# Kernel tuning notes

Measured on AMD Instinct MI355X. Metric: run time of the kernel, lower is better.

## Reference

```python
import jax, jax.numpy as jnp
import numpy as np

N = 20000
E = 320000
IN_DIM = 512
HID = 64
HEADS = 8
OUT_DIM = 40
NEG_SLOPE = 0.2


def glorot(key, shape):
    fan = shape[0] + shape[-1] if len(shape) > 1 else shape[-1]
    s = jnp.sqrt(6.0 / fan)
    return jax.random.uniform(key, shape, jnp.float32, -s, s)


def setup_inputs() -> dict:
    key = jax.random.key(0)
    ks = jax.random.split(key, 12)
    x = jax.random.normal(ks[0], (N, IN_DIM), jnp.float32)
    edge_index = jax.random.randint(ks[1], (2, E), 0, N, jnp.int64)
    return {
        "x": x,
        "edge_index": edge_index,
        "W1": glorot(ks[2], (IN_DIM, HEADS * HID)),
        "att1_src": glorot(ks[3], (HEADS, HID)),
        "att1_dst": glorot(ks[4], (HEADS, HID)),
        "b1": jnp.zeros((HEADS * HID,), jnp.float32),
        "W2": glorot(ks[5], (HEADS * HID, HEADS * HID)),
        "att2_src": glorot(ks[6], (HEADS, HID)),
        "att2_dst": glorot(ks[7], (HEADS, HID)),
        "b2": jnp.zeros((HEADS * HID,), jnp.float32),
        "W3": glorot(ks[8], (HEADS * HID, OUT_DIM)),
        "att3_src": glorot(ks[9], (1, OUT_DIM)),
        "att3_dst": glorot(ks[10], (1, OUT_DIM)),
        "b3": jnp.zeros((OUT_DIM,), jnp.float32),
    }


def gat_conv(x, src, dst, W, att_src, att_dst, bias, heads, out_c):
    # h: [N, H, C] transformed node features
    h = (x @ W).reshape(N, heads, out_c)
    a_src = jnp.sum(h * att_src, axis=-1)  # [N, H]
    a_dst = jnp.sum(h * att_dst, axis=-1)  # [N, H]
    # edge logits (message j=src -> i=dst), softmax grouped by dst
    logits = jax.nn.leaky_relu(a_src[src] + a_dst[dst], NEG_SLOPE)  # [Etot, H]
    seg_max = jax.ops.segment_max(logits, dst, num_segments=N)
    seg_max = jnp.where(jnp.isfinite(seg_max), seg_max, 0.0)
    ex = jnp.exp(logits - seg_max[dst])
    denom = jax.ops.segment_sum(ex, dst, num_segments=N)
    alpha = ex / (denom[dst] + 1e-16)  # [Etot, H]
    msg = h[src] * alpha[:, :, None]  # [Etot, H, C]
    out = jax.ops.segment_sum(msg, dst, num_segments=N)  # [N, H, C]
    return out.reshape(N, heads * out_c) + bias


def reference(x, edge_index, W1, att1_src, att1_dst, b1,
              W2, att2_src, att2_dst, b2,
              W3, att3_src, att3_dst, b3):
    # add self loops (PyG GATConv default)
    loops = jnp.arange(N, dtype=edge_index.dtype)
    src = jnp.concatenate([edge_index[0], loops])
    dst = jnp.concatenate([edge_index[1], loops])
    # dropout layers are identity in eval mode
    h = jax.nn.elu(gat_conv(x, src, dst, W1, att1_src, att1_dst, b1, HEADS, HID))
    h = jax.nn.elu(gat_conv(h, src, dst, W2, att2_src, att2_dst, b2, HEADS, HID))
    h = gat_conv(h, src, dst, W3, att3_src, att3_dst, b3, 1, OUT_DIM)
    return jax.nn.log_softmax(h, axis=-1)
```

## Files before the change

kernel.cpp:

```cpp
#include <hip/hip_runtime.h>
#include <math.h>

#define NN 20000
#define EE 320000
#define ETOT (EE + NN)
#define NEG 0.2f

typedef unsigned short ushortT;
typedef __attribute__((ext_vector_type(8))) short short8v;
typedef __attribute__((ext_vector_type(8))) unsigned short u16x8;
typedef __attribute__((ext_vector_type(4))) float f32x4;

__device__ __forceinline__ ushortT f2b(float f){
  unsigned u = __float_as_uint(f);
  u += 0x7FFFu + ((u >> 16) & 1u);
  return (ushortT)(u >> 16);
}
__device__ __forceinline__ float b2f(ushortT b){
  return __uint_as_float(((unsigned)b) << 16);
}

__global__ void k_cvt(const float* __restrict__ in, ushortT* __restrict__ outp, int n4){
  int i = blockIdx.x*blockDim.x + threadIdx.x;
  if(i < n4){
    float4 v = *reinterpret_cast<const float4*>(in + (size_t)i*4);
    ushort4 o;
    o.x = f2b(v.x); o.y = f2b(v.y); o.z = f2b(v.z); o.w = f2b(v.w);
    *reinterpret_cast<ushort4*>(outp + (size_t)i*4) = o;
  }
}

__global__ void k_wtrans(const float* __restrict__ W, ushortT* __restrict__ Wt){
  __shared__ float t[32][33];
  int bk = blockIdx.x*32, bn = blockIdx.y*32;
  int tx = threadIdx.x & 31, ty = threadIdx.x >> 5;
  for(int r=0;r<32;r+=8)
    t[ty+r][tx] = W[(size_t)(bk+ty+r)*512 + bn+tx];
  __syncthreads();
  for(int r=0;r<32;r+=8)
    Wt[(size_t)(bn+ty+r)*512 + bk+tx] = f2b(t[tx][ty+r]);
}

__global__ void k_wtrans3(const float* __restrict__ W3, ushortT* __restrict__ Wt3p){
  int idx = blockIdx.x*blockDim.x + threadIdx.x;
  if(idx >= 64*48*8) return;
  int kslot = idx / 384;
  int rem = idx - kslot*384;
  int n = rem >> 3;
  int jj = rem & 7;
  int k = kslot*8 + jj;
  float v = (n < 40) ? W3[(size_t)k*40 + n] : 0.f;
  Wt3p[idx] = f2b(v);
}

__global__ void k_count(const int* __restrict__ edst, int* __restrict__ counts){
  int e = blockIdx.x*blockDim.x + threadIdx.x;
  if(e < ETOT){
    int d = (e < EE) ? edst[e] : (e - EE);
    atomicAdd(&counts[d], 1);
  }
}

__global__ void k_scan(const int* __restrict__ counts, int* __restrict__ rowstart){
  __shared__ int lds[1024];
  int tid = threadIdx.x;
  int base = tid*20;
  int s = 0;
  for(int j=0;j<20;j++){ int i=base+j; if(i<NN) s += counts[i]; }
  lds[tid] = s; __syncthreads();
  for(int off=1; off<1024; off<<=1){
    int v = (tid>=off) ? lds[tid-off] : 0;
    __syncthreads();
    lds[tid] += v;
    __syncthreads();
  }
  int run = lds[tid] - s;
  for(int j=0;j<20;j++){
    int i = base+j;
    if(i <= NN){
      rowstart[i] = run;
      if(i < NN) run += counts[i];
    }
  }
}

__global__ void k_fill(const int* __restrict__ esrc, const int* __restrict__ edst,
                       const int* __restrict__ rowstart,
                       int* __restrict__ cursor, int* __restrict__ srcs){
  int e = blockIdx.x*blockDim.x + threadIdx.x;
  if(e < ETOT){
    int d = (e < EE) ? edst[e] : (e - EE);
    int s = (e < EE) ? esrc[e] : (e - EE);
    int pos = rowstart[d] + atomicAdd(&cursor[d], 1);
    srcs[pos] = s;
  }
}

__global__ __launch_bounds__(256) void k_gemm_bf16(
    const ushortT* __restrict__ A, const ushortT* __restrict__ Bt,
    ushortT* __restrict__ Cb, int M)
{
  const int K = 512;
  __shared__ __align__(16) ushortT As[128*32];
  __shared__ __align__(16) ushortT Bs[128*32];
  int bm = blockIdx.x*128, bn = blockIdx.y*128;
  int tid = threadIdx.x, wave = tid>>6, lane = tid&63;
  int wm = (wave>>1)*64, wn = (wave&1)*64;
  f32x4 acc[4][4] = {};

  int l4 = lane>>2;
  int s4 = lane&3;
  int src_slot = s4 ^ (l4 & 3);
  int r16 = lane&15, kg = lane>>4;

  for(int k0=0;k0<K;k0+=32){
    #pragma unroll
    for(int c=0;c<2;c++){
      int chunk = wave*2 + c;
      int arow = bm + chunk*16 + l4; if(arow > M-1) arow = M-1;
      const ushortT* ga = A + (size_t)arow*K + k0 + src_slot*8;
      __builtin_amdgcn_global_load_lds(
          (const __attribute__((address_space(1))) void*)ga,
          (__attribute__((address_space(3))) void*)(As + chunk*16*32), 16, 0, 0);
      int brow = bn + chunk*16 + l4;
      const ushortT* gb = Bt + (size_t)brow*K + k0 + src_slot*8;
      __builtin_amdgcn_global_load_lds(
          (const __attribute__((address_space(1))) void*)gb,
          (__attribute__((address_space(3))) void*)(Bs + chunk*16*32), 16, 0, 0);
    }
    asm volatile("s_waitcnt vmcnt(0)");
    __syncthreads();

    short8v a_frag[4], b_frag[4];
    #pragma unroll
    for(int i=0;i<4;i++){
      int row = wm + i*16 + r16;
      a_frag[i] = *reinterpret_cast<const short8v*>(As + row*32 + ((kg ^ (row&3))<<3));
    }
    #pragma unroll
    for(int j=0;j<4;j++){
      int row = wn + j*16 + r16;
      b_frag[j] = *reinterpret_cast<const short8v*>(Bs + row*32 + ((kg ^ (row&3))<<3));
    }
    #pragma unroll
    for(int i=0;i<4;i++)
      #pragma unroll
      for(int j=0;j<4;j++)
        acc[i][j] = __builtin_amdgcn_mfma_f32_16x16x32_bf16(a_frag[i], b_frag[j], acc[i][j], 0, 0, 0);
    __syncthreads();
  }

  #pragma unroll
  for(int i=0;i<4;i++){
    #pragma unroll
    for(int j=0;j<4;j++){
      #pragma unroll
      for(int r=0;r<4;r++){
        int row = bm + wm + i*16 + kg*4 + r;
        int col = bn + wn + j*16 + r16;
        if(row < M) Cb[(size_t)row*512 + col] = f2b(acc[i][j][r]);
      }
    }
  }
}

__global__ __launch_bounds__(256) void k_gemm3m(const ushortT* __restrict__ A,
                                                const ushortT* __restrict__ Wt3p,
                                                float* __restrict__ C, int M){
  const int K = 512;
  __shared__ __align__(16) ushortT As[128*32];
  __shared__ __align__(16) ushortT Bs[64*48*8];
  int bm = blockIdx.x*128;
  int tid = threadIdx.x, wave = tid>>6, lane = tid&63;

  #pragma unroll
  for(int it=0; it<12; it++){
    int o = (it*256 + tid)*8;
    *reinterpret_cast<u16x8*>(Bs + o) = *reinterpret_cast<const u16x8*>(Wt3p + o);
  }

  int l4 = lane>>2, s4 = lane&3;
  int src_slot = s4 ^ (l4 & 3);
  int r16 = lane&15, kg = lane>>4;
  f32x4 acc[2][3] = {};

  for(int k0=0;k0<K;k0+=32){
    #pragma unroll
    for(int c=0;c<2;c++){
      int chunk = wave*2 + c;
      int arow = bm + chunk*16 + l4; if(arow > M-1) arow = M-1;
      const ushortT* ga = A + (size_t)arow*K + k0 + src_slot*8;
      __builtin_amdgcn_global_load_lds(
          (const __attribute__((address_space(1))) void*)ga,
          (__attribute__((address_space(3))) void*)(As + chunk*16*32), 16, 0, 0);
    }
    asm volatile("s_waitcnt vmcnt(0)");
    __syncthreads();

    short8v a_frag[2], b_frag[3];
    #pragma unroll
    for(int i=0;i<2;i++){
      int row = wave*32 + i*16 + r16;
      a_frag[i] = *reinterpret_cast<const short8v*>(As + row*32 + ((kg ^ (row&3))<<3));
    }
    int kslot = (k0>>3) + kg;
    #pragma unroll
    for(int j=0;j<3;j++){
      b_frag[j] = *reinterpret_cast<const short8v*>(Bs + kslot*384 + (j*16 + r16)*8);
    }
    #pragma unroll
    for(int i=0;i<2;i++)
      #pragma unroll
      for(int j=0;j<3;j++)
        acc[i][j] = __builtin_amdgcn_mfma_f32_16x16x32_bf16(a_frag[i], b_frag[j], acc[i][j], 0, 0, 0);
    __syncthreads();
  }

  #pragma unroll
  for(int i=0;i<2;i++){
    #pragma unroll
    for(int j=0;j<3;j++){
      #pragma unroll
      for(int r=0;r<4;r++){
        int row = bm + wave*32 + i*16 + kg*4 + r;
        int col = j*16 + r16;
        if(row < M && col < 40) C[(size_t)row*40 + col] = acc[i][j][r];
      }
    }
  }
}

__global__ void k_attn8(const ushortT* __restrict__ feat, const float* __restrict__ atts,
                        const float* __restrict__ attd, float* __restrict__ a_s,
                        float* __restrict__ a_d){
  int n = blockIdx.x*4 + (threadIdx.x>>6);
  int lane = threadIdx.x & 63;
  if(n >= NN) return;
  int c0 = lane*8;
  u16x8 v = *reinterpret_cast<const u16x8*>(feat + (size_t)n*512 + c0);
  float s1 = 0.f, s2 = 0.f;
  #pragma unroll
  for(int j=0;j<8;j++){
    float f = b2f((ushortT)v[j]);
    s1 += f*atts[c0+j];
    s2 += f*attd[c0+j];
  }
  #pragma unroll
  for(int off=1; off<8; off<<=1){
    s1 += __shfl_xor(s1, off);
    s2 += __shfl_xor(s2, off);
  }
  if((lane&7) == 0){
    int head = lane>>3;
    a_s[n*8+head] = s1;
    a_d[n*8+head] = s2;
  }
}

template<int H, int C>
__global__ void k_attn_f(const float* __restrict__ feat, const float* __restrict__ atts,
                         const float* __restrict__ attd, float* __restrict__ a_s,
                         float* __restrict__ a_d){
  int n = blockIdx.x*4 + (threadIdx.x>>6);
  int lane = threadIdx.x & 63;
  if(n >= NN) return;
  #pragma unroll
  for(int h=0;h<H;h++){
    float s1 = 0.f, s2 = 0.f;
    if(lane < C){
      float v = feat[(size_t)n*(H*C) + h*C + lane];
      s1 = v*atts[h*C+lane];
      s2 = v*attd[h*C+lane];
    }
    for(int off=32; off; off>>=1){
      s1 += __shfl_xor(s1, off);
      s2 += __shfl_xor(s2, off);
    }
    if(lane == 0){ a_s[n*H+h] = s1; a_d[n*H+h] = s2; }
  }
}

__global__ __launch_bounds__(256) void k_agg512(const ushortT* __restrict__ feat,
    const float* __restrict__ a_s, const float* __restrict__ a_d,
    const int* __restrict__ rowstart, const int* __restrict__ srcs,
    const float* __restrict__ bias, ushortT* __restrict__ outb){
  int d = blockIdx.x*4 + (threadIdx.x>>6);
  int lane = threadIdx.x & 63;
  unsigned c0 = (unsigned)lane*8u;
  int head = lane>>3;
  float ad_h = a_d[(size_t)d*8 + head];
  float acc[8] = {0.f,0.f,0.f,0.f,0.f,0.f,0.f,0.f};
  float dsum = 0.f;
  int p0 = rowstart[d], p1 = rowstart[d+1];
  int p = p0;

  for(; p+8 <= p1; p += 8){
    int   ss[8];
    float ll[8];
    u16x8 vv[8];
    #pragma unroll
    for(int q=0;q<8;q++) ss[q] = srcs[p+q];
    #pragma unroll
    for(int q=0;q<8;q++) ll[q] = a_s[((unsigned)ss[q]<<3) + (unsigned)head];
    #pragma unroll
    for(int q=0;q<8;q++) vv[q] = *reinterpret_cast<const u16x8*>(feat + (((unsigned)ss[q]<<9) + c0));
    #pragma unroll
    for(int q=0;q<8;q++){
      float l  = ll[q] + ad_h;
      float al = __expf(fmaxf(l, NEG*l));
      dsum += al;
      #pragma unroll
      for(int j=0;j<8;j++) acc[j] += al*b2f((ushortT)vv[q][j]);
    }
  }
  for(; p+4 <= p1; p += 4){
    int   ss[4];
    float ll[4];
    u16x8 vv[4];
    #pragma unroll
    for(int q=0;q<4;q++) ss[q] = srcs[p+q];
    #pragma unroll
    for(int q=0;q<4;q++) ll[q] = a_s[((unsigned)ss[q]<<3) + (unsigned)head];
    #pragma unroll
    for(int q=0;q<4;q++) vv[q] = *reinterpret_cast<const u16x8*>(feat + (((unsigned)ss[q]<<9) + c0));
    #pragma unroll
    for(int q=0;q<4;q++){
      float l  = ll[q] + ad_h;
      float al = __expf(fmaxf(l, NEG*l));
      dsum += al;
      #pragma unroll
      for(int j=0;j<8;j++) acc[j] += al*b2f((ushortT)vv[q][j]);
    }
  }
  for(; p<p1; p++){
    int s_ = srcs[p];
    float l = a_s[((unsigned)s_<<3) + (unsigned)head] + ad_h;
    u16x8 v = *reinterpret_cast<const u16x8*>(feat + (((unsigned)s_<<9) + c0));
    float al = __expf(fmaxf(l, NEG*l));
    dsum += al;
    #pragma unroll
    for(int j=0;j<8;j++) acc[j] += al*b2f((ushortT)v[j]);
  }

  float invd = 1.f/(dsum + 1e-16f);
  u16x8 ov;
  #pragma unroll
  for(int j=0;j<8;j++){
    float o = acc[j]*invd + bias[c0+j];
    o = (o > 0.f) ? o : (__expf(o) - 1.f);
    ov[j] = f2b(o);
  }
  *reinterpret_cast<u16x8*>(outb + (size_t)d*512 + c0) = ov;
}

__global__ void k_agg_l3(const float* __restrict__ feat,
    const float* __restrict__ a_s, const float* __restrict__ a_d,
    const int* __restrict__ rowstart, const int* __restrict__ srcs,
    const float* __restrict__ bias, float* __restrict__ outp){
  int d = blockIdx.x;
  int lane = threadIdx.x;
  bool act = lane < 40;
  int li = act ? lane : 0;
  float ad_v = a_d[d];
  float acc = 0.f, dsum = 0.f;
  int p0 = rowstart[d], p1 = rowstart[d+1];
  int p = p0;
  for(; p+4 <= p1; p += 4){
    int s0_ = srcs[p], s1_ = srcs[p+1], s2_ = srcs[p+2], s3_ = srcs[p+3];
    float l0 = a_s[s0_] + ad_v, l1 = a_s[s1_] + ad_v;
    float l2 = a_s[s2_] + ad_v, l3 = a_s[s3_] + ad_v;
    float v0 = feat[(size_t)s0_*40 + li];
    float v1 = feat[(size_t)s1_*40 + li];
    float v2 = feat[(size_t)s2_*40 + li];
    float v3 = feat[(size_t)s3_*40 + li];
    float al0 = __expf(fmaxf(l0, NEG*l0));
    float al1 = __expf(fmaxf(l1, NEG*l1));
    float al2 = __expf(fmaxf(l2, NEG*l2));
    float al3 = __expf(fmaxf(l3, NEG*l3));
    dsum += al0 + al1 + al2 + al3;
    acc += al0*v0 + al1*v1 + al2*v2 + al3*v3;
  }
  for(; p<p1; p++){
    int s_ = srcs[p];
    float l = a_s[s_] + ad_v;
    float al = __expf(fmaxf(l, NEG*l));
    dsum += al;
    acc += al*feat[(size_t)s_*40 + li];
  }
  float invd = 1.f/(dsum + 1e-16f);
  float o = act ? (acc*invd + bias[lane]) : -1e30f;
  float m = o;
  for(int off=32; off; off>>=1) m = fmaxf(m, __shfl_xor(m, off));
  float e_ = act ? expf(o - m) : 0.f;
  float ssum = e_;
  for(int off=32; off; off>>=1) ssum += __shfl_xor(ssum, off);
  if(act) outp[(size_t)d*40 + lane] = o - m - logf(ssum);
}

extern "C" void kernel_launch(void* const* d_in, const int* in_sizes, int n_in,
                              void* d_out, int out_size, void* d_ws, size_t ws_size,
                              hipStream_t stream){
  const float* x   = (const float*)d_in[0];
  const int*   ei  = (const int*)d_in[1];
  const int*   esrc = ei;
  const int*   edst = ei + EE;
  const float* W1  = (const float*)d_in[2];
  const float* as1 = (const float*)d_in[3];
  const float* ad1 = (const float*)d_in[4];
  const float* b1  = (const float*)d_in[5];
  const float* W2  = (const float*)d_in[6];
  const float* as2 = (const float*)d_in[7];
  const float* ad2 = (const float*)d_in[8];
  const float* b2  = (const float*)d_in[9];
  const float* W3  = (const float*)d_in[10];
  const float* as3 = (const float*)d_in[11];
  const float* ad3 = (const float*)d_in[12];
  const float* b3  = (const float*)d_in[13];
  float* out = (float*)d_out;

  char* w = (char*)d_ws;
  size_t off = 0;
  auto alloc = [&](size_t bytes)->char*{
    char* p = w + off;
    off = (off + bytes + 255) & ~(size_t)255;
    return p;
  };
  ushortT*  xb   = (ushortT*)alloc((size_t)NN*512*2);
  ushortT*  fA   = (ushortT*)alloc((size_t)NN*512*2);
  ushortT*  fB   = (ushortT*)alloc((size_t)NN*512*2);
  float*    h3   = (float*)alloc((size_t)NN*40*4);
  ushortT*  Wt1  = (ushortT*)alloc((size_t)512*512*2);
  ushortT*  Wt2  = (ushortT*)alloc((size_t)512*512*2);
  ushortT*  Wt3p = (ushortT*)alloc((size_t)64*48*8*2);
  float*    a_s  = (float*)alloc((size_t)NN*8*4);
  float*    a_d  = (float*)alloc((size_t)NN*8*4);
  int* rowstart  = (int*)alloc((size_t)(NN+1)*4);
  int* cursor    = (int*)alloc((size_t)NN*4);
  int* counts    = (int*)alloc((size_t)NN*4);
  int* srcs      = (int*)alloc((size_t)ETOT*4);

  k_cvt<<<(NN*512/4 + 255)/256, 256, 0, stream>>>(x, xb, NN*512/4);
  dim3 wt_grid(16, 16);
  k_wtrans<<<wt_grid, 256, 0, stream>>>(W1, Wt1);
  k_wtrans<<<wt_grid, 256, 0, stream>>>(W2, Wt2);
  k_wtrans3<<<(64*48*8 + 255)/256, 256, 0, stream>>>(W3, Wt3p);

  hipMemsetAsync(counts, 0, (size_t)NN*4, stream);
  hipMemsetAsync(cursor, 0, (size_t)NN*4, stream);
  k_count<<<(ETOT+255)/256, 256, 0, stream>>>(edst, counts);
  k_scan<<<1, 1024, 0, stream>>>(counts, rowstart);
  k_fill<<<(ETOT+255)/256, 256, 0, stream>>>(esrc, edst, rowstart, cursor, srcs);

  dim3 mgrid((NN+127)/128, 4);

  k_gemm_bf16<<<mgrid, 256, 0, stream>>>(xb, Wt1, fA, NN);
  k_attn8<<<(NN+3)/4, 256, 0, stream>>>(fA, as1, ad1, a_s, a_d);
  k_agg512<<<NN/4, 256, 0, stream>>>(fA, a_s, a_d, rowstart, srcs, b1, fB);

  k_gemm_bf16<<<mgrid, 256, 0, stream>>>(fB, Wt2, fA, NN);
  k_attn8<<<(NN+3)/4, 256, 0, stream>>>(fA, as2, ad2, a_s, a_d);
  k_agg512<<<NN/4, 256, 0, stream>>>(fA, a_s, a_d, rowstart, srcs, b2, fB);

  k_gemm3m<<<(NN+127)/128, 256, 0, stream>>>(fB, Wt3p, h3, NN);
  k_attn_f<1,40><<<(NN+3)/4, 256, 0, stream>>>(h3, as3, ad3, a_s, a_d);
  k_agg_l3<<<NN, 64, 0, stream>>>(h3, a_s, a_d, rowstart, srcs, b3, out);
}
```

Baseline: 272.3 us.

## Split 512-feature aggregation into per-head slices with edge-parallel lanes

The layer-1/2 aggregation kernel now uses 8 waves per block, each handling one destination node for a single head slice (64 channels). Lanes split into 8 edge groups times 8 channel groups, so each wave handles 8 edges in parallel. Partial sums are then combined with cross-lane shuffles before the bias, ELU and bf16 store. The goal is more parallelism and memory-level concurrency per destination, replacing one wave per node that walked edges serially. In exchange it adds shuffle-reduction overhead, idle lanes on nodes with few edges, and many more blocks.

```diff
diff --git a/kernel.cpp b/kernel.cpp
--- a/kernel.cpp
+++ b/kernel.cpp
@@ -280,77 +280,51 @@
   }
 }
 
-__global__ __launch_bounds__(256) void k_agg512(const ushortT* __restrict__ feat,
+__global__ __launch_bounds__(512) void k_agg512(const ushortT* __restrict__ feat,
     const float* __restrict__ a_s, const float* __restrict__ a_d,
     const int* __restrict__ rowstart, const int* __restrict__ srcs,
     const float* __restrict__ bias, ushortT* __restrict__ outb){
-  int d = blockIdx.x*4 + (threadIdx.x>>6);
-  int lane = threadIdx.x & 63;
-  unsigned c0 = (unsigned)lane*8u;
-  int head = lane>>3;
-  float ad_h = a_d[(size_t)d*8 + head];
+  int wave = threadIdx.x>>6;
+  int lane = threadIdx.x&63;
+  int slice = blockIdx.x & 7;
+  int d = ((blockIdx.x>>3)<<3) + wave;
+  int eg = lane>>3, cg = lane&7;
+  unsigned cbase = ((unsigned)slice<<6) + ((unsigned)cg<<3);
+  float ad_h = a_d[((unsigned)d<<3) + slice];
   float acc[8] = {0.f,0.f,0.f,0.f,0.f,0.f,0.f,0.f};
   float dsum = 0.f;
   int p0 = rowstart[d], p1 = rowstart[d+1];
-  int p = p0;
-
-  for(; p+8 <= p1; p += 8){
-    int   ss[8];
-    float ll[8];
-    u16x8 vv[8];
-    #pragma unroll
-    for(int q=0;q<8;q++) ss[q] = srcs[p+q];
-    #pragma unroll
-    for(int q=0;q<8;q++) ll[q] = a_s[((unsigned)ss[q]<<3) + (unsigned)head];
-    #pragma unroll
-    for(int q=0;q<8;q++) vv[q] = *reinterpret_cast<const u16x8*>(feat + (((unsigned)ss[q]<<9) + c0));
-    #pragma unroll
-    for(int q=0;q<8;q++){
-      float l  = ll[q] + ad_h;
-      float al = __expf(fmaxf(l, NEG*l));
-      dsum += al;
-      #pragma unroll
-      for(int j=0;j<8;j++) acc[j] += al*b2f((ushortT)vv[q][j]);
-    }
-  }
-  for(; p+4 <= p1; p += 4){
-    int   ss[4];
-    float ll[4];
-    u16x8 vv[4];
-    #pragma unroll
-    for(int q=0;q<4;q++) ss[q] = srcs[p+q];
-    #pragma unroll
-    for(int q=0;q<4;q++) ll[q] = a_s[((unsigned)ss[q]<<3) + (unsigned)head];
-    #pragma unroll
-    for(int q=0;q<4;q++) vv[q] = *reinterpret_cast<const u16x8*>(feat + (((unsigned)ss[q]<<9) + c0));
-    #pragma unroll
-    for(int q=0;q<4;q++){
-      float l  = ll[q] + ad_h;
-      float al = __expf(fmaxf(l, NEG*l));
-      dsum += al;
-      #pragma unroll
-      for(int j=0;j<8;j++) acc[j] += al*b2f((ushortT)vv[q][j]);
-    }
-  }
-  for(; p<p1; p++){
-    int s_ = srcs[p];
-    float l = a_s[((unsigned)s_<<3) + (unsigned)head] + ad_h;
-    u16x8 v = *reinterpret_cast<const u16x8*>(feat + (((unsigned)s_<<9) + c0));
-    float al = __expf(fmaxf(l, NEG*l));
+
+  for(int p = p0; p < p1; p += 8){
+    int pe = p + eg;
+    bool valid = pe < p1;
+    int s_ = srcs[valid ? pe : (p1-1)];
+    float l = a_s[((unsigned)s_<<3) + slice] + ad_h;
+    u16x8 v = *reinterpret_cast<const u16x8*>(feat + (((unsigned)s_<<9) + cbase));
+    float al = valid ? __expf(fmaxf(l, NEG*l)) : 0.f;
     dsum += al;
     #pragma unroll
     for(int j=0;j<8;j++) acc[j] += al*b2f((ushortT)v[j]);
   }
 
-  float invd = 1.f/(dsum + 1e-16f);
-  u16x8 ov;
-  #pragma unroll
-  for(int j=0;j<8;j++){
-    float o = acc[j]*invd + bias[c0+j];
-    o = (o > 0.f) ? o : (__expf(o) - 1.f);
-    ov[j] = f2b(o);
-  }
-  *reinterpret_cast<u16x8*>(outb + (size_t)d*512 + c0) = ov;
+  #pragma unroll
+  for(int off=8; off<64; off<<=1){
+    dsum += __shfl_xor(dsum, off);
+    #pragma unroll
+    for(int j=0;j<8;j++) acc[j] += __shfl_xor(acc[j], off);
+  }
+
+  if(eg == 0){
+    float invd = 1.f/(dsum + 1e-16f);
+    u16x8 ov;
+    #pragma unroll
+    for(int j=0;j<8;j++){
+      float o = acc[j]*invd + bias[cbase+j];
+      o = (o > 0.f) ? o : (__expf(o) - 1.f);
+      ov[j] = f2b(o);
+    }
+    *reinterpret_cast<u16x8*>(outb + (size_t)d*512 + cbase) = ov;
+  }
 }
 
 __global__ void k_agg_l3(const float* __restrict__ feat,
@@ -455,11 +429,11 @@
 
   k_gemm_bf16<<<mgrid, 256, 0, stream>>>(xb, Wt1, fA, NN);
   k_attn8<<<(NN+3)/4, 256, 0, stream>>>(fA, as1, ad1, a_s, a_d);
-  k_agg512<<<NN/4, 256, 0, stream>>>(fA, a_s, a_d, rowstart, srcs, b1, fB);
+  k_agg512<<<NN, 512, 0, stream>>>(fA, a_s, a_d, rowstart, srcs, b1, fB);
 
   k_gemm_bf16<<<mgrid, 256, 0, stream>>>(fB, Wt2, fA, NN);
   k_attn8<<<(NN+3)/4, 256, 0, stream>>>(fA, as2, ad2, a_s, a_d);
-  k_agg512<<<NN/4, 256, 0, stream>>>(fA, a_s, a_d, rowstart, srcs, b2, fB);
+  k_agg512<<<NN, 512, 0, stream>>>(fA, a_s, a_d, rowstart, srcs, b2, fB);
 
   k_gemm3m<<<(NN+127)/128, 256, 0, stream>>>(fB, Wt3p, h3, NN);
   k_attn_f<1,40><<<(NN+3)/4, 256, 0, stream>>>(h3, as3, ad3, a_s, a_d);
```

Result: slower. 316.1 us (+16.1%).
